# Optimization experiments

Hardware: AMD Instinct MI355X
Metric: run time of the kernel (lower is better)

Reference implementation:

```python
import jax, jax.numpy as jnp
import numpy as np

EPS = 1e-6

def _phi(x):
    # elu_feature_map: elu(x) + 1 (positive feature map)
    return jax.nn.elu(x) + 1.0

def setup_inputs() -> dict:
    key = jax.random.key(0)
    ks = jax.random.split(key, 6)
    N, L, S, H, E, D = 4, 2048, 2048, 16, 64, 64
    return {
        "queries1": jax.random.normal(ks[0], (N, L, H, E), jnp.float32),
        "keys1": jax.random.normal(ks[1], (N, S, H, E), jnp.float32),
        "values1": jax.random.normal(ks[2], (N, S, H, D), jnp.float32),
        "queries2": jax.random.normal(ks[3], (N, L, H, E), jnp.float32),
        "keys2": jax.random.normal(ks[4], (N, S, H, E), jnp.float32),
        "values2": jax.random.normal(ks[5], (N, S, H, D), jnp.float32),
        "key_lengths1": jnp.ones((N, S), jnp.float32),
        "key_lengths2": jnp.ones((N, S), jnp.float32),
    }

def _linear_cross(Q, K_other, V_other):
    # Q: (N,L,H,E) featurized queries; K_other: (N,S,H,E) featurized+masked keys
    # KV: (N,H,D,E) ; 'nshd,nshm->nhmd'
    KV = jnp.einsum('nshd,nshm->nhmd', K_other, V_other)
    Ksum = K_other.sum(axis=1)                      # (N,H,E)
    Z = 1.0 / (jnp.einsum('nlhd,nhd->nlh', Q, Ksum) + EPS)
    # 'nlhd,nhmd,nlh->nlhm'
    return jnp.einsum('nlhd,nhmd->nlhm', Q, KV) * Z[..., None]

def reference(queries1, keys1, values1, queries2, keys2, values2,
              key_lengths1, key_lengths2):
    Q1 = _phi(queries1)
    K1 = _phi(keys1) * key_lengths1[:, :, None, None]
    Q2 = _phi(queries2)
    K2 = _phi(keys2) * key_lengths2[:, :, None, None]
    V1 = _linear_cross(Q1, K2, values2)  # stream1 queries attend to stream2 keys/values
    V2 = _linear_cross(Q2, K1, values1)  # stream2 queries attend to stream1 keys/values
    return (V1, V2)
```

## Files before the change

kernel.cpp:

```cpp
#include <hip/hip_runtime.h>

#define NB 4
#define LL 2048
#define SS 2048
#define HH 16
#define EE 64
#define DD 64

#define NHEAD (2*NB*HH)
#define NCHUNK 8
#define KVP ((size_t)NHEAD*NCHUNK*4096)
#define WSFLOATS (KVP + (size_t)NHEAD*NCHUNK*64)

typedef short short8 __attribute__((ext_vector_type(8)));
typedef float floatx4 __attribute__((ext_vector_type(4)));

__device__ inline float phi(float x) { return x > 0.f ? x + 1.f : __expf(x); }

__device__ inline unsigned int f2bf(float f) {
    unsigned int x = __float_as_uint(f);
    return (x + 0x7FFFu + ((x >> 16) & 1u)) >> 16;
}
__device__ inline void split_pack(float a, float b, unsigned int &hp, unsigned int &lp) {
    const unsigned int ha = f2bf(a), hb = f2bf(b);
    const float ra = a - __uint_as_float(ha << 16);
    const float rb = b - __uint_as_float(hb << 16);
    hp = (ha & 0xFFFFu) | (hb << 16);
    lp = (f2bf(ra) & 0xFFFFu) | (f2bf(rb) << 16);
}

__device__ inline int swz(int row, int col) {
    return ((((col >> 3) ^ ((row >> 2) ^ row)) & 7) << 3) | (col & 7);
}

__global__ __launch_bounds__(256) void kv_kernel(
    const float* __restrict__ k1, const float* __restrict__ v1,
    const float* __restrict__ k2, const float* __restrict__ v2,
    const float* __restrict__ kl1, const float* __restrict__ kl2,
    float* __restrict__ ws)
{
    const int b = blockIdx.x;
    const int chunk = b & 7;
    const int h = (b >> 3) & 15;
    const int n = (b >> 7) & 3;
    const int st = (b >> 9) & 1;
    const float* K  = st ? k1 : k2;
    const float* V  = st ? v1 : v2;
    const float* KL = st ? kl1 : kl2;

    __shared__ __align__(16) unsigned short KtH[64][64];
    __shared__ __align__(16) unsigned short KtL[64][64];
    __shared__ __align__(16) unsigned short VtH[64][64];
    __shared__ __align__(16) unsigned short VtL[64][64];

    const int t = threadIdx.x;
    const int lane = t & 63;
    const int w = t >> 6;
    const int d4 = t & 15;
    const int sp = t >> 4;
    const int c = lane & 15;
    const int q = lane >> 4;

    float ksum[4] = {0.f, 0.f, 0.f, 0.f};
    floatx4 acc[4];
#pragma unroll
    for (int i = 0; i < 4; i++) acc[i] = (floatx4){0.f, 0.f, 0.f, 0.f};

    float4 cur[8]; float curl[4];
    {
        const int sbase = chunk * 256;
#pragma unroll
        for (int i = 0; i < 2; ++i) {
            const int sl = 2 * sp + 32 * i;
            const size_t off = ((size_t)((size_t)n * SS + sbase + sl) * HH + h) * EE + 4 * d4;
            cur[4 * i + 0] = *(const float4*)&K[off];
            cur[4 * i + 1] = *(const float4*)&K[off + HH * EE];
            cur[4 * i + 2] = *(const float4*)&V[off];
            cur[4 * i + 3] = *(const float4*)&V[off + HH * EE];
            curl[2 * i + 0] = KL[(size_t)n * SS + sbase + sl];
            curl[2 * i + 1] = KL[(size_t)n * SS + sbase + sl + 1];
        }
    }

    for (int g = 0; g < 4; ++g) {
        float4 nxt[8]; float nxtl[4];
        if (g < 3) {
            const int sbase = chunk * 256 + (g + 1) * 64;
#pragma unroll
            for (int i = 0; i < 2; ++i) {
                const int sl = 2 * sp + 32 * i;
                const size_t off = ((size_t)((size_t)n * SS + sbase + sl) * HH + h) * EE + 4 * d4;
                nxt[4 * i + 0] = *(const float4*)&K[off];
                nxt[4 * i + 1] = *(const float4*)&K[off + HH * EE];
                nxt[4 * i + 2] = *(const float4*)&V[off];
                nxt[4 * i + 3] = *(const float4*)&V[off + HH * EE];
                nxtl[2 * i + 0] = KL[(size_t)n * SS + sbase + sl];
                nxtl[2 * i + 1] = KL[(size_t)n * SS + sbase + sl + 1];
            }
        }
        if (g) __syncthreads();
#pragma unroll
        for (int i = 0; i < 2; ++i) {
            const int sl = 2 * sp + 32 * i;
            const float4 ka = cur[4 * i + 0], kb = cur[4 * i + 1];
            const float4 va = cur[4 * i + 2], vb = cur[4 * i + 3];
            const float l0 = curl[2 * i + 0], l1 = curl[2 * i + 1];
            const float a0 = phi(ka.x) * l0, a1 = phi(ka.y) * l0;
            const float a2 = phi(ka.z) * l0, a3 = phi(ka.w) * l0;
            const float b0 = phi(kb.x) * l1, b1 = phi(kb.y) * l1;
            const float b2 = phi(kb.z) * l1, b3 = phi(kb.w) * l1;
            ksum[0] += a0 + b0; ksum[1] += a1 + b1;
            ksum[2] += a2 + b2; ksum[3] += a3 + b3;
            unsigned int hp, lp;
            const int r0 = 4 * d4;
            const int s0 = swz(r0 + 0, sl), s1 = swz(r0 + 1, sl);
            const int s2 = swz(r0 + 2, sl), s3 = swz(r0 + 3, sl);
            split_pack(a0, b0, hp, lp);
            *(unsigned int*)&KtH[r0 + 0][s0] = hp; *(unsigned int*)&KtL[r0 + 0][s0] = lp;
            split_pack(a1, b1, hp, lp);
            *(unsigned int*)&KtH[r0 + 1][s1] = hp; *(unsigned int*)&KtL[r0 + 1][s1] = lp;
            split_pack(a2, b2, hp, lp);
            *(unsigned int*)&KtH[r0 + 2][s2] = hp; *(unsigned int*)&KtL[r0 + 2][s2] = lp;
            split_pack(a3, b3, hp, lp);
            *(unsigned int*)&KtH[r0 + 3][s3] = hp; *(unsigned int*)&KtL[r0 + 3][s3] = lp;
            split_pack(va.x, vb.x, hp, lp);
            *(unsigned int*)&VtH[r0 + 0][s0] = hp; *(unsigned int*)&VtL[r0 + 0][s0] = lp;
            split_pack(va.y, vb.y, hp, lp);
            *(unsigned int*)&VtH[r0 + 1][s1] = hp; *(unsigned int*)&VtL[r0 + 1][s1] = lp;
            split_pack(va.z, vb.z, hp, lp);
            *(unsigned int*)&VtH[r0 + 2][s2] = hp; *(unsigned int*)&VtL[r0 + 2][s2] = lp;
            split_pack(va.w, vb.w, hp, lp);
            *(unsigned int*)&VtH[r0 + 3][s3] = hp; *(unsigned int*)&VtL[r0 + 3][s3] = lp;
        }
        __syncthreads();
        const int ra = 16 * w + c;
#pragma unroll
        for (int ks = 0; ks < 2; ++ks) {
            const int ca = swz(ra, 32 * ks + 8 * q);
            const short8 aH = *(const short8*)&VtH[ra][ca];
            const short8 aL = *(const short8*)&VtL[ra][ca];
#pragma unroll
            for (int dt = 0; dt < 4; ++dt) {
                const int rb = 16 * dt + c;
                const int cb = swz(rb, 32 * ks + 8 * q);
                const short8 bH = *(const short8*)&KtH[rb][cb];
                const short8 bL = *(const short8*)&KtL[rb][cb];
                acc[dt] = __builtin_amdgcn_mfma_f32_16x16x32_bf16(aH, bH, acc[dt], 0, 0, 0);
                acc[dt] = __builtin_amdgcn_mfma_f32_16x16x32_bf16(aH, bL, acc[dt], 0, 0, 0);
                acc[dt] = __builtin_amdgcn_mfma_f32_16x16x32_bf16(aL, bH, acc[dt], 0, 0, 0);
            }
        }
        if (g < 3) {
#pragma unroll
            for (int i = 0; i < 8; ++i) cur[i] = nxt[i];
#pragma unroll
            for (int i = 0; i < 4; ++i) curl[i] = nxtl[i];
        }
    }

    const int head = (st * NB + n) * HH + h;
    const size_t kvbase = ((size_t)head * NCHUNK + chunk) * 4096;
#pragma unroll
    for (int dt = 0; dt < 4; ++dt)
#pragma unroll
        for (int r = 0; r < 4; ++r)
            ws[kvbase + (size_t)(16 * w + 4 * q + r) * 64 + 16 * dt + c] = acc[dt][r];

    float (*scr)[64] = (float(*)[64])VtL;
    __syncthreads();
    scr[sp][4 * d4 + 0] = ksum[0];
    scr[sp][4 * d4 + 1] = ksum[1];
    scr[sp][4 * d4 + 2] = ksum[2];
    scr[sp][4 * d4 + 3] = ksum[3];
    __syncthreads();
    if (t < 64) {
        float s = 0.f;
#pragma unroll
        for (int i = 0; i < 16; ++i) s += scr[i][t];
        ws[KVP + ((size_t)head * NCHUNK + chunk) * 64 + t] = s;
    }
}

__global__ __launch_bounds__(256) void reduce_kernel(float* __restrict__ ws)
{
    const int head = blockIdx.x;
    const int t = threadIdx.x;
    const size_t base = (size_t)head * (NCHUNK * 4096);
    const int m = t >> 2;
    const int dbase = (t & 3) * 16;

    float4 kv[4];
#pragma unroll
    for (int i = 0; i < 4; ++i) {
        const int d0 = dbase + 4 * i;
        const size_t eo = (size_t)m * 64 + d0;
        float4 s = *(const float4*)&ws[base + eo];
#pragma unroll
        for (int ch = 1; ch < NCHUNK; ++ch) {
            const float4 p = *(const float4*)&ws[base + (size_t)ch * 4096 + eo];
            s.x += p.x; s.y += p.y; s.z += p.z; s.w += p.w;
        }
        kv[i] = s;
    }
    float ks = 0.f;
    if (t < 64) {
#pragma unroll
        for (int ch = 0; ch < NCHUNK; ++ch)
            ks += ws[KVP + ((size_t)head * NCHUNK + ch) * 64 + t];
    }
    __syncthreads();

    const int fm = ((m >> 2) ^ m) & 7;
    unsigned int* W = (unsigned int*)&ws[base];
#pragma unroll
    for (int i = 0; i < 4; ++i) {
        const int d0 = dbase + 4 * i;
        const int bp = ((((d0 >> 3) ^ fm) & 7) << 2) + ((d0 & 4) >> 1);
        unsigned int hp, lp;
        split_pack(kv[i].x, kv[i].y, hp, lp);
        W[m * 32 + bp]     = hp;  W[2048 + m * 32 + bp]     = lp;
        split_pack(kv[i].z, kv[i].w, hp, lp);
        W[m * 32 + bp + 1] = hp;  W[2048 + m * 32 + bp + 1] = lp;
    }
    if (t < 64) ws[KVP + (size_t)head * NCHUNK * 64 + t] = ks;
}

static __device__ __forceinline__ float lt_body(
    const float4 qa0, const float4 qb0, const float4 qa1, const float4 qb1,
    const float* Ksp,
    const unsigned short (*BH)[64], const unsigned short (*BL)[64],
    const int c, const int q, floatx4* acc)
{
    float z = 0.f;
#pragma unroll
    for (int ks = 0; ks < 2; ++ks) {
        const float4 qa = ks ? qa1 : qa0;
        const float4 qb = ks ? qb1 : qb0;
        const int co = 32 * ks + 8 * q;
        const float p[8] = {phi(qa.x), phi(qa.y), phi(qa.z), phi(qa.w),
                            phi(qb.x), phi(qb.y), phi(qb.z), phi(qb.w)};
        z += p[0] * Ksp[co + 0] + p[1] * Ksp[co + 1]
           + p[2] * Ksp[co + 2] + p[3] * Ksp[co + 3]
           + p[4] * Ksp[co + 4] + p[5] * Ksp[co + 5]
           + p[6] * Ksp[co + 6] + p[7] * Ksp[co + 7];
        short8 aH, aL;
#pragma unroll
        for (int j = 0; j < 8; ++j) {
            const unsigned int hb = f2bf(p[j]);
            aH[j] = (short)hb;
            aL[j] = (short)f2bf(p[j] - __uint_as_float(hb << 16));
        }
#pragma unroll
        for (int mt = 0; mt < 4; ++mt) {
            const int rb = 16 * mt + c;
            const int cb = swz(rb, co);
            const short8 bH = *(const short8*)&BH[rb][cb];
            const short8 bL = *(const short8*)&BL[rb][cb];
            acc[mt] = __builtin_amdgcn_mfma_f32_16x16x32_bf16(aH, bH, acc[mt], 0, 0, 0);
            acc[mt] = __builtin_amdgcn_mfma_f32_16x16x32_bf16(aH, bL, acc[mt], 0, 0, 0);
            acc[mt] = __builtin_amdgcn_mfma_f32_16x16x32_bf16(aL, bH, acc[mt], 0, 0, 0);
        }
    }
    return z;
}

__global__ __launch_bounds__(256) void out_kernel(
    const float* __restrict__ q1, const float* __restrict__ q2,
    const float* __restrict__ ws, float* __restrict__ out)
{
    const int b = blockIdx.x;
    const int lc = b & 15;
    const int h = (b >> 4) & 15;
    const int n = (b >> 8) & 3;
    const int st = (b >> 10) & 1;
    const float* Q = st ? q2 : q1;
    float* O = out + (size_t)st * ((size_t)NB * LL * HH * DD);

    __shared__ __align__(16) unsigned short BtH[64][64];
    __shared__ __align__(16) unsigned short BtL[64][64];
    __shared__ float Ks[64];

    const int t = threadIdx.x;
    const int lane = t & 63;
    const int w = t >> 6;
    const int c = lane & 15;
    const int q = lane >> 4;
    const int head = (st * NB + n) * HH + h;
    const int lbase = lc * 128;

    const float* qr0 = &Q[((size_t)((size_t)n * LL + lbase + 32 * w + c) * HH + h) * EE];
    const int d0q = 8 * q;
    const float4 p00 = *(const float4*)&qr0[d0q];
    const float4 p01 = *(const float4*)&qr0[d0q + 4];
    const float4 p02 = *(const float4*)&qr0[d0q + 32];
    const float4 p03 = *(const float4*)&qr0[d0q + 36];
    const float* qr1 = qr0 + (size_t)16 * HH * EE;
    const float4 p10 = *(const float4*)&qr1[d0q];
    const float4 p11 = *(const float4*)&qr1[d0q + 4];
    const float4 p12 = *(const float4*)&qr1[d0q + 32];
    const float4 p13 = *(const float4*)&qr1[d0q + 36];

    {
        const uint4* src = (const uint4*)(ws + (size_t)head * (NCHUNK * 4096));
        uint4* dstH = (uint4*)&BtH[0][0];
        uint4* dstL = (uint4*)&BtL[0][0];
        dstH[t]       = src[t];
        dstH[t + 256] = src[t + 256];
        dstL[t]       = src[512 + t];
        dstL[t + 256] = src[768 + t];
    }
    if (t < 64) Ks[t] = ws[KVP + (size_t)head * NCHUNK * 64 + t];
    __syncthreads();

    floatx4 acc[8];
#pragma unroll
    for (int i = 0; i < 8; ++i) acc[i] = (floatx4){0.f, 0.f, 0.f, 0.f};

    float z0 = lt_body(p00, p01, p02, p03, Ks, BtH, BtL, c, q, acc);
    float z1 = lt_body(p10, p11, p12, p13, Ks, BtH, BtL, c, q, acc + 4);

    z0 += __shfl_xor(z0, 16); z0 += __shfl_xor(z0, 32);
    z1 += __shfl_xor(z1, 16); z1 += __shfl_xor(z1, 32);
    const float zi0 = 1.f / (z0 + 1e-6f);
    const float zi1 = 1.f / (z1 + 1e-6f);

#pragma unroll
    for (int lt = 0; lt < 2; ++lt) {
        const float zi = lt ? zi1 : zi0;
#pragma unroll
        for (int r = 0; r < 4; ++r) {
            const float zz = __shfl(zi, 4 * q + r);
            const int ll = 32 * w + 16 * lt + 4 * q + r;
            const size_t ro = ((size_t)((size_t)n * LL + lbase + ll) * HH + h) * DD;
#pragma unroll
            for (int mt = 0; mt < 4; ++mt)
                O[ro + 16 * mt + c] = acc[4 * lt + mt][r] * zz;
        }
    }
}

extern "C" void kernel_launch(void* const* d_in, const int* in_sizes, int n_in,
                              void* d_out, int out_size, void* d_ws, size_t ws_size,
                              hipStream_t stream) {
    const float* q1  = (const float*)d_in[0];
    const float* k1  = (const float*)d_in[1];
    const float* v1  = (const float*)d_in[2];
    const float* q2  = (const float*)d_in[3];
    const float* k2  = (const float*)d_in[4];
    const float* v2  = (const float*)d_in[5];
    const float* kl1 = (const float*)d_in[6];
    const float* kl2 = (const float*)d_in[7];
    float* ws = (float*)d_ws;
    float* out = (float*)d_out;

    kv_kernel<<<dim3(1024), dim3(256), 0, stream>>>(k1, v1, k2, v2, kl1, kl2, ws);
    reduce_kernel<<<dim3(128), dim3(256), 0, stream>>>(ws);
    out_kernel<<<dim3(2048), dim3(256), 0, stream>>>(q1, q2, ws, out);
}
```

Measured before the change: 240.8 us.

## Double KV chunking, spread reduction over more blocks, use hardware bf16 pack conversion

Splits the sequence into 16 chunks instead of 8, so the KV partial-product kernel launches twice as many blocks, each covering a shorter stretch. The reduction now uses four blocks per head instead of one and writes packed bf16 hi/lo KV into a separate output region, which removes the in-place overwrite and its barrier. Software bf16 rounding is replaced with the v_cvt_pk_bf16_f32 instruction in both the reduction and the output kernel's query split. In exchange, the workspace and the partial-sum traffic grow, and each block's shorter loop gives less load/compute overlap.

```diff
diff --git a/kernel.cpp b/kernel.cpp
--- a/kernel.cpp
+++ b/kernel.cpp
@@ -8,25 +8,23 @@
 #define DD 64
 
 #define NHEAD (2*NB*HH)
-#define NCHUNK 8
-#define KVP ((size_t)NHEAD*NCHUNK*4096)
-#define WSFLOATS (KVP + (size_t)NHEAD*NCHUNK*64)
+#define NCHUNK 16
+#define KVP   ((size_t)NHEAD*NCHUNK*4096)
+#define KVOUT (KVP + (size_t)NHEAD*NCHUNK*64)
+#define WSFLOATS (KVOUT + (size_t)NHEAD*4096)
 
 typedef short short8 __attribute__((ext_vector_type(8)));
 typedef float floatx4 __attribute__((ext_vector_type(4)));
 
 __device__ inline float phi(float x) { return x > 0.f ? x + 1.f : __expf(x); }
 
-__device__ inline unsigned int f2bf(float f) {
-    unsigned int x = __float_as_uint(f);
-    return (x + 0x7FFFu + ((x >> 16) & 1u)) >> 16;
-}
 __device__ inline void split_pack(float a, float b, unsigned int &hp, unsigned int &lp) {
-    const unsigned int ha = f2bf(a), hb = f2bf(b);
-    const float ra = a - __uint_as_float(ha << 16);
-    const float rb = b - __uint_as_float(hb << 16);
-    hp = (ha & 0xFFFFu) | (hb << 16);
-    lp = (f2bf(ra) & 0xFFFFu) | (f2bf(rb) << 16);
+    unsigned int h, l;
+    asm("v_cvt_pk_bf16_f32 %0, %1, %2" : "=v"(h) : "v"(a), "v"(b));
+    const float ra = a - __uint_as_float(h << 16);
+    const float rb = b - __uint_as_float(h & 0xFFFF0000u);
+    asm("v_cvt_pk_bf16_f32 %0, %1, %2" : "=v"(l) : "v"(ra), "v"(rb));
+    hp = h; lp = l;
 }
 
 __device__ inline int swz(int row, int col) {
@@ -40,10 +38,10 @@
     float* __restrict__ ws)
 {
     const int b = blockIdx.x;
-    const int chunk = b & 7;
-    const int h = (b >> 3) & 15;
-    const int n = (b >> 7) & 3;
-    const int st = (b >> 9) & 1;
+    const int chunk = b & 15;
+    const int h = (b >> 4) & 15;
+    const int n = (b >> 8) & 3;
+    const int st = (b >> 10) & 1;
     const float* K  = st ? k1 : k2;
     const float* V  = st ? v1 : v2;
     const float* KL = st ? kl1 : kl2;
@@ -68,7 +66,7 @@
 
     float4 cur[8]; float curl[4];
     {
-        const int sbase = chunk * 256;
+        const int sbase = chunk * 128;
 #pragma unroll
         for (int i = 0; i < 2; ++i) {
             const int sl = 2 * sp + 32 * i;
@@ -82,10 +80,10 @@
         }
     }
 
-    for (int g = 0; g < 4; ++g) {
+    for (int g = 0; g < 2; ++g) {
         float4 nxt[8]; float nxtl[4];
-        if (g < 3) {
-            const int sbase = chunk * 256 + (g + 1) * 64;
+        if (g < 1) {
+            const int sbase = chunk * 128 + 64;
 #pragma unroll
             for (int i = 0; i < 2; ++i) {
                 const int sl = 2 * sp + 32 * i;
@@ -150,7 +148,7 @@
                 acc[dt] = __builtin_amdgcn_mfma_f32_16x16x32_bf16(aL, bH, acc[dt], 0, 0, 0);
             }
         }
-        if (g < 3) {
+        if (g < 1) {
 #pragma unroll
             for (int i = 0; i < 8; ++i) cur[i] = nxt[i];
 #pragma unroll
@@ -183,46 +181,38 @@
 
 __global__ __launch_bounds__(256) void reduce_kernel(float* __restrict__ ws)
 {
-    const int head = blockIdx.x;
+    const int bq = blockIdx.x;
+    const int head = bq >> 2;
+    const int qt = bq & 3;
     const int t = threadIdx.x;
     const size_t base = (size_t)head * (NCHUNK * 4096);
-    const int m = t >> 2;
-    const int dbase = (t & 3) * 16;
-
-    float4 kv[4];
-#pragma unroll
-    for (int i = 0; i < 4; ++i) {
-        const int d0 = dbase + 4 * i;
-        const size_t eo = (size_t)m * 64 + d0;
-        float4 s = *(const float4*)&ws[base + eo];
-#pragma unroll
-        for (int ch = 1; ch < NCHUNK; ++ch) {
-            const float4 p = *(const float4*)&ws[base + (size_t)ch * 4096 + eo];
-            s.x += p.x; s.y += p.y; s.z += p.z; s.w += p.w;
-        }
-        kv[i] = s;
-    }
-    float ks = 0.f;
-    if (t < 64) {
+    const int m = qt * 16 + (t >> 4);
+    const int d0 = (t & 15) * 4;
+    const size_t eo = (size_t)m * 64 + d0;
+
+    float4 s = *(const float4*)&ws[base + eo];
+#pragma unroll
+    for (int ch = 1; ch < NCHUNK; ++ch) {
+        const float4 p = *(const float4*)&ws[base + (size_t)ch * 4096 + eo];
+        s.x += p.x; s.y += p.y; s.z += p.z; s.w += p.w;
+    }
+
+    const int fm = ((m >> 2) ^ m) & 7;
+    unsigned int* W = (unsigned int*)&ws[KVOUT + (size_t)head * 4096];
+    const int bp = ((((d0 >> 3) ^ fm) & 7) << 2) + ((d0 & 4) >> 1);
+    unsigned int hp, lp;
+    split_pack(s.x, s.y, hp, lp);
+    W[m * 32 + bp]     = hp;  W[2048 + m * 32 + bp]     = lp;
+    split_pack(s.z, s.w, hp, lp);
+    W[m * 32 + bp + 1] = hp;  W[2048 + m * 32 + bp + 1] = lp;
+
+    if (qt == 0 && t < 64) {
+        float ks = 0.f;
 #pragma unroll
         for (int ch = 0; ch < NCHUNK; ++ch)
             ks += ws[KVP + ((size_t)head * NCHUNK + ch) * 64 + t];
-    }
-    __syncthreads();
-
-    const int fm = ((m >> 2) ^ m) & 7;
-    unsigned int* W = (unsigned int*)&ws[base];
-#pragma unroll
-    for (int i = 0; i < 4; ++i) {
-        const int d0 = dbase + 4 * i;
-        const int bp = ((((d0 >> 3) ^ fm) & 7) << 2) + ((d0 & 4) >> 1);
-        unsigned int hp, lp;
-        split_pack(kv[i].x, kv[i].y, hp, lp);
-        W[m * 32 + bp]     = hp;  W[2048 + m * 32 + bp]     = lp;
-        split_pack(kv[i].z, kv[i].w, hp, lp);
-        W[m * 32 + bp + 1] = hp;  W[2048 + m * 32 + bp + 1] = lp;
-    }
-    if (t < 64) ws[KVP + (size_t)head * NCHUNK * 64 + t] = ks;
+        ws[KVP + (size_t)head * NCHUNK * 64 + t] = ks;
+    }
 }
 
 static __device__ __forceinline__ float lt_body(
@@ -244,11 +234,13 @@
            + p[4] * Ksp[co + 4] + p[5] * Ksp[co + 5]
            + p[6] * Ksp[co + 6] + p[7] * Ksp[co + 7];
         short8 aH, aL;
-#pragma unroll
-        for (int j = 0; j < 8; ++j) {
-            const unsigned int hb = f2bf(p[j]);
-            aH[j] = (short)hb;
-            aL[j] = (short)f2bf(p[j] - __uint_as_float(hb << 16));
+        unsigned int* ah = (unsigned int*)&aH;
+        unsigned int* al = (unsigned int*)&aL;
+#pragma unroll
+        for (int j = 0; j < 4; ++j) {
+            unsigned int hp, lp;
+            split_pack(p[2 * j], p[2 * j + 1], hp, lp);
+            ah[j] = hp; al[j] = lp;
         }
 #pragma unroll
         for (int mt = 0; mt < 4; ++mt) {
@@ -301,7 +293,7 @@
     const float4 p13 = *(const float4*)&qr1[d0q + 36];
 
     {
-        const uint4* src = (const uint4*)(ws + (size_t)head * (NCHUNK * 4096));
+        const uint4* src = (const uint4*)(ws + KVOUT + (size_t)head * 4096);
         uint4* dstH = (uint4*)&BtH[0][0];
         uint4* dstL = (uint4*)&BtL[0][0];
         dstH[t]       = src[t];
@@ -353,7 +345,7 @@
     float* ws = (float*)d_ws;
     float* out = (float*)d_out;
 
-    kv_kernel<<<dim3(1024), dim3(256), 0, stream>>>(k1, v1, k2, v2, kl1, kl2, ws);
-    reduce_kernel<<<dim3(128), dim3(256), 0, stream>>>(ws);
+    kv_kernel<<<dim3(2048), dim3(256), 0, stream>>>(k1, v1, k2, v2, kl1, kl2, ws);
+    reduce_kernel<<<dim3(512), dim3(256), 0, stream>>>(ws);
     out_kernel<<<dim3(2048), dim3(256), 0, stream>>>(q1, q2, ws, out);
 }
```

After: 248.9 us. +3.3%, slower.
